# Optimization experiments

Measured on AMD Instinct MI355X. Metric: run time of the kernel, lower is better.

## Reference

```python
import jax, jax.numpy as jnp
import numpy as np

N_NODES = 50000
NEG_SLOPE = 0.2


def gat_layer(x, src, dst, edge_attr, W, a_src, a_dst, We, a_edge, b, n):
    """PyG GATConv (heads=1, concat=True, add_self_loops=True, fill_value='mean')."""
    h = x @ W                                   # [N, C] shared lin for src/dst
    alpha_s = h @ a_src                          # [N]
    alpha_d = h @ a_dst                          # [N]
    # self loops; self-loop edge_attr = mean of incoming edge_attr per node
    deg = jax.ops.segment_sum(jnp.ones_like(dst, dtype=edge_attr.dtype), dst, num_segments=n)
    ea_mean = jax.ops.segment_sum(edge_attr, dst, num_segments=n) / jnp.maximum(deg, 1.0)[:, None]
    loop = jnp.arange(n, dtype=src.dtype)
    s = jnp.concatenate([src, loop])             # [E+N]
    d = jnp.concatenate([dst, loop])
    ea = jnp.concatenate([edge_attr, ea_mean], axis=0)
    alpha_e = (ea @ We) @ a_edge                 # [E+N]
    alpha = jax.nn.leaky_relu(alpha_s[s] + alpha_d[d] + alpha_e, NEG_SLOPE)
    # segment softmax over destination neighborhoods (self-loops guarantee non-empty)
    amax = jax.ops.segment_max(alpha, d, num_segments=n)
    ealpha = jnp.exp(alpha - amax[d])
    denom = jax.ops.segment_sum(ealpha, d, num_segments=n)
    coef = ealpha / denom[d]                     # [E+N]
    out = jax.ops.segment_sum(h[s] * coef[:, None], d, num_segments=n)
    return out + b


def setup_inputs() -> dict:
    key = jax.random.key(0)
    ks = jax.random.split(key, 16)
    N, E, F_in, H, C, ED = N_NODES, 800000, 256, 128, 128, 60
    inp = {
        "x": jax.random.normal(ks[0], (N, F_in), jnp.float32),
        "edge_index": jax.random.randint(ks[1], (2, E), 0, N, jnp.int32),
        "edge_features": jax.random.normal(ks[2], (E, ED), jnp.float32),
        "batch_size": 16,
    }
    def glorot(k, shape):
        fan = shape[0] + (shape[1] if len(shape) > 1 else 1)
        return jax.random.normal(k, shape, jnp.float32) * np.sqrt(2.0 / fan)
    # layer 1
    inp["W1"] = glorot(ks[3], (F_in, H))
    inp["a_src1"] = glorot(ks[4], (H,))
    inp["a_dst1"] = glorot(ks[5], (H,))
    inp["We1"] = glorot(ks[6], (ED, H))
    inp["a_edge1"] = glorot(ks[7], (H,))
    inp["b1"] = jnp.zeros((H,), jnp.float32)
    # layer 2
    inp["W2"] = glorot(ks[8], (H, C))
    inp["a_src2"] = glorot(ks[9], (C,))
    inp["a_dst2"] = glorot(ks[10], (C,))
    inp["We2"] = glorot(ks[11], (ED, C))
    inp["a_edge2"] = glorot(ks[12], (C,))
    inp["b2"] = jnp.zeros((C,), jnp.float32)
    return inp


def reference(x, edge_index, edge_features, batch_size,
              W1, a_src1, a_dst1, We1, a_edge1, b1,
              W2, a_src2, a_dst2, We2, a_edge2, b2):
    n = x.shape[0]
    src, dst = edge_index[0], edge_index[1]
    h = gat_layer(x, src, dst, edge_features, W1, a_src1, a_dst1, We1, a_edge1, b1, n)
    h = jax.nn.relu(h)
    z = gat_layer(h, src, dst, edge_features, W2, a_src2, a_dst2, We2, a_edge2, b2, n)
    # decode: gather-dot over labeled edge pairs
    res = jnp.sum(z[src] * z[dst], axis=-1)      # [E]
    half = res.shape[0] // 2
    res_half = res[:half] + res[half:]
    return res_half.reshape((batch_size, -1))
```

## Files before the change

kernel.cpp:

```cpp
#include <hip/hip_runtime.h>
#include <hip/hip_bf16.h>

typedef __attribute__((ext_vector_type(8))) short short8;
typedef __attribute__((ext_vector_type(4))) float floatx4;

__device__ __forceinline__ float lrelu(float a){ return a > 0.f ? a : 0.2f * a; }
__device__ __forceinline__ float bflo(unsigned u){ return __uint_as_float(u << 16); }
__device__ __forceinline__ float bfhi(unsigned u){ return __uint_as_float(u & 0xffff0000u); }
__device__ __forceinline__ unsigned short f2bf(float f){
  __hip_bfloat16 h = __float2bfloat16(f);
  return *reinterpret_cast<unsigned short*>(&h);
}
__device__ __forceinline__ float dot4(float4 a, float4 b){
  return a.x*b.x + a.y*b.y + a.z*b.z + a.w*b.w;
}

__global__ __launch_bounds__(256) void k_prep(const int* __restrict__ dst, int* __restrict__ degi,
                       int* __restrict__ eslot, int E, int CB,
                       const float* __restrict__ We1, const float* __restrict__ ae1,
                       const float* __restrict__ We2, const float* __restrict__ ae2,
                       float* __restrict__ we1, float* __restrict__ we2,
                       const float* __restrict__ W1, unsigned short* __restrict__ W1t,
                       const float* __restrict__ W2, unsigned short* __restrict__ W2t) {
  int t = threadIdx.x;
  if (blockIdx.x < (unsigned)CB) {
    int e = blockIdx.x * 256 + t;
    if (e < E) eslot[e] = atomicAdd(degi + dst[e], 1);
    return;
  }
  int b = blockIdx.x - CB;
  if (b == 0) {
    if (t >= 64) return;
    float s1 = 0.f, s2 = 0.f;
    if (t < 60) {
      const float4* r1 = reinterpret_cast<const float4*>(We1 + t * 128);
      const float4* r2 = reinterpret_cast<const float4*>(We2 + t * 128);
      const float4* a1 = reinterpret_cast<const float4*>(ae1);
      const float4* a2 = reinterpret_cast<const float4*>(ae2);
      for (int i = 0; i < 32; ++i) {
        float4 x1 = r1[i], y1 = a1[i];
        float4 x2 = r2[i], y2 = a2[i];
        s1 += x1.x*y1.x + x1.y*y1.y + x1.z*y1.z + x1.w*y1.w;
        s2 += x2.x*y2.x + x2.y*y2.y + x2.z*y2.z + x2.w*y2.w;
      }
    }
    we1[t] = s1; we2[t] = s2;
  } else if (b <= 128) {
    int idx = (b - 1) * 256 + t;
    int k = idx >> 7, n = idx & 127;
    W1t[(size_t)n * 256 + k] = f2bf(W1[idx]);
  } else {
    int idx = (b - 129) * 256 + t;
    int k = idx >> 7, n = idx & 127;
    W2t[(size_t)n * 128 + k] = f2bf(W2[idx]);
  }
}

__device__ __forceinline__ void scan_body(const int* __restrict__ degi, int* __restrict__ rowptr,
                                          int N, int E) {
  __shared__ int wsums[16];
  int t = threadIdx.x;
  int wave = t >> 6, lane = t & 63;
  const int CH = 52;
  int lo = t * CH;
  int v[52];
  int s = 0;
  #pragma unroll
  for (int i = 0; i < 13; ++i) {
    int base_i = lo + 4 * i;
    if (base_i + 4 <= N) {
      int4 q = *reinterpret_cast<const int4*>(degi + base_i);
      v[4*i+0] = q.x; v[4*i+1] = q.y; v[4*i+2] = q.z; v[4*i+3] = q.w;
      s += q.x + q.y + q.z + q.w;
    } else {
      #pragma unroll
      for (int j = 0; j < 4; ++j) {
        int idx = base_i + j;
        int x = (idx < N) ? degi[idx] : 0;
        v[4*i+j] = x; s += x;
      }
    }
  }
  int inc = s;
  #pragma unroll
  for (int off = 1; off < 64; off <<= 1) {
    int u = __shfl_up(inc, off);
    if (lane >= off) inc += u;
  }
  if (lane == 63) wsums[wave] = inc;
  __syncthreads();
  if (wave == 0) {
    int ws = (lane < 16) ? wsums[lane] : 0;
    #pragma unroll
    for (int off = 1; off < 16; off <<= 1) {
      int u = __shfl_up(ws, off);
      if (lane >= off) ws += u;
    }
    if (lane < 16) wsums[lane] = ws;
  }
  __syncthreads();
  int base = inc - s + (wave ? wsums[wave - 1] : 0);
  #pragma unroll
  for (int i = 0; i < 13; ++i) {
    int base_i = lo + 4 * i;
    if (base_i + 4 <= N) {
      int4 o;
      o.x = base; base += v[4*i+0];
      o.y = base; base += v[4*i+1];
      o.z = base; base += v[4*i+2];
      o.w = base; base += v[4*i+3];
      *reinterpret_cast<int4*>(rowptr + base_i) = o;
    } else {
      #pragma unroll
      for (int j = 0; j < 4; ++j) {
        int idx = base_i + j;
        if (idx < N) { rowptr[idx] = base; base += v[4*i+j]; }
      }
    }
  }
  if (t == 0) rowptr[N] = E;
}

__global__ __launch_bounds__(1024) void k_scanedot(const int* __restrict__ degi, int* __restrict__ rowptr,
                       int N, int E,
                       const float* __restrict__ ef,
                       const float* __restrict__ we1, const float* __restrict__ we2,
                       float2* __restrict__ edgeD, int EDOTB) {
  if (blockIdx.x == 0) { scan_body(degi, rowptr, N, E); return; }
  int t = threadIdx.x;
  int sub = t & 3;
  int qw = (int)(blockIdx.x - 1) * 256 + (t >> 2);
  const float4* w1v = reinterpret_cast<const float4*>(we1);
  const float4* w2v = reinterpret_cast<const float4*>(we2);
  float4 wa0 = w1v[sub],     wb0 = w2v[sub];
  float4 wa1 = w1v[sub + 4], wb1 = w2v[sub + 4];
  float4 wa2 = w1v[sub + 8], wb2 = w2v[sub + 8];
  bool has3 = sub < 3;
  float4 wa3 = make_float4(0.f,0.f,0.f,0.f), wb3 = wa3;
  if (has3) { wa3 = w1v[sub + 12]; wb3 = w2v[sub + 12]; }
  const float4* efq = reinterpret_cast<const float4*>(ef);
  int stride = EDOTB * 256;
  for (int e = qw; e < E; e += stride) {
    size_t b = (size_t)e * 15;
    float4 f0 = efq[b + sub];
    float4 f1 = efq[b + sub + 4];
    float4 f2 = efq[b + sub + 8];
    float4 f3 = make_float4(0.f,0.f,0.f,0.f);
    if (has3) f3 = efq[b + sub + 12];
    float d1 = dot4(f0, wa0) + dot4(f1, wa1) + dot4(f2, wa2) + dot4(f3, wa3);
    float d2 = dot4(f0, wb0) + dot4(f1, wb1) + dot4(f2, wb2) + dot4(f3, wb3);
    d1 += __shfl_xor(d1, 1); d1 += __shfl_xor(d1, 2);
    d2 += __shfl_xor(d2, 1); d2 += __shfl_xor(d2, 2);
    if (sub == 0) edgeD[e] = make_float2(d1, d2);
  }
}

template <int K, bool AFP32>
__device__ __forceinline__ void gemm_body(int wid, int lane,
    const void* __restrict__ Av, const unsigned short* __restrict__ Bt,
    unsigned short* __restrict__ C,
    const float* __restrict__ a_src, const float* __restrict__ a_dst,
    float* __restrict__ alps, float* __restrict__ alpd, int M) {
  int mt = wid;
  if (mt * 16 >= M) return;
  int r = lane & 15, quad = lane >> 4;
  int m = mt * 16 + r;
  floatx4 acc[8] = {};
  for (int k0 = 0; k0 < K; k0 += 32) {
    int kk = k0 + quad * 8;
    short8 a;
    if (AFP32) {
      const float4* ap = reinterpret_cast<const float4*>((const float*)Av + (size_t)m * K + kk);
      float4 lo = ap[0], hi = ap[1];
      union { short8 v; unsigned short u[8]; } pa;
      pa.u[0]=f2bf(lo.x); pa.u[1]=f2bf(lo.y); pa.u[2]=f2bf(lo.z); pa.u[3]=f2bf(lo.w);
      pa.u[4]=f2bf(hi.x); pa.u[5]=f2bf(hi.y); pa.u[6]=f2bf(hi.z); pa.u[7]=f2bf(hi.w);
      a = pa.v;
    } else {
      a = *reinterpret_cast<const short8*>((const unsigned short*)Av + (size_t)m * K + kk);
    }
    #pragma unroll
    for (int t = 0; t < 8; ++t) {
      short8 b = *reinterpret_cast<const short8*>(Bt + (size_t)(t*16 + r) * K + kk);
      acc[t] = __builtin_amdgcn_mfma_f32_16x16x32_bf16(a, b, acc[t], 0, 0, 0);
    }
  }
  float asv[8], adv[8];
  #pragma unroll
  for (int t = 0; t < 8; ++t) {
    int col = t * 16 + r;
    asv[t] = a_src[col]; adv[t] = a_dst[col];
  }
  #pragma unroll
  for (int rr = 0; rr < 4; ++rr) {
    float ps = 0.f, pd = 0.f;
    #pragma unroll
    for (int t = 0; t < 8; ++t) { ps += acc[t][rr] * asv[t]; pd += acc[t][rr] * adv[t]; }
    #pragma unroll
    for (int mo = 1; mo <= 8; mo <<= 1) { ps += __shfl_xor(ps, mo); pd += __shfl_xor(pd, mo); }
    if (r == 0) {
      int row = mt * 16 + quad * 4 + rr;
      alps[row] = ps;
      alpd[row] = pd;
    }
  }
  #pragma unroll
  for (int t = 0; t < 8; ++t) {
    int col = t * 16 + r;
    #pragma unroll
    for (int rr = 0; rr < 4; ++rr) {
      int row = mt * 16 + quad * 4 + rr;
      C[(size_t)row * 128 + col] = f2bf(acc[t][rr]);
    }
  }
}

template <int K, bool AFP32>
__global__ __launch_bounds__(256) void k_gemm(const void* __restrict__ Av, const unsigned short* __restrict__ Bt,
                                              unsigned short* __restrict__ C,
                                              const float* __restrict__ a_src, const float* __restrict__ a_dst,
                                              float* __restrict__ alps, float* __restrict__ alpd, int M) {
  int wid = (blockIdx.x * 256 + threadIdx.x) >> 6;
  int lane = threadIdx.x & 63;
  gemm_body<K, AFP32>(wid, lane, Av, Bt, C, a_src, a_dst, alps, alpd, M);
}

__global__ __launch_bounds__(256) void k_scatgemm(
                       const int* __restrict__ src, const int* __restrict__ dst,
                       const int* __restrict__ eslot, const int* __restrict__ rowptr,
                       const float2* __restrict__ edgeD, float4* __restrict__ csr,
                       int E, int GB,
                       const float* __restrict__ x, const unsigned short* __restrict__ W1t,
                       unsigned short* __restrict__ hA,
                       const float* __restrict__ a_src, const float* __restrict__ a_dst,
                       float* __restrict__ alps, float* __restrict__ alpd, int N) {
  int t = threadIdx.x;
  if (blockIdx.x < (unsigned)GB) {
    int wid = (blockIdx.x * 256 + t) >> 6;
    int lane = t & 63;
    gemm_body<256, true>(wid, lane, x, W1t, hA, a_src, a_dst, alps, alpd, N);
    return;
  }
  int e = (blockIdx.x - GB) * 256 + t;
  if (e >= E) return;
  int d = dst[e];
  float2 dd = edgeD[e];
  int slot = rowptr[d] + eslot[e];
  float4 v;
  v.x = __int_as_float(src[e]); v.y = dd.x; v.z = dd.y; v.w = 0.f;
  csr[slot] = v;
}

__global__ __launch_bounds__(256) void k_agg(const int* __restrict__ rowptr, const float4* __restrict__ csr,
                      const float* __restrict__ as_, const float* __restrict__ ad_,
                      const unsigned short* __restrict__ h, const float* __restrict__ bias,
                      unsigned short* __restrict__ out, int N, int use2, int do_relu) {
  int i = (blockIdx.x * blockDim.x + threadIdx.x) >> 6;
  int lane = threadIdx.x & 63;
  if (i >= N) return;
  int st = lane >> 4;
  int q  = lane & 15;
  int start = rowptr[i], end = rowptr[i + 1];
  int cnt = end - start;
  float adi = ad_[i], asi = as_[i];
  float m = -3.0e38f, s = 0.f, esum = 0.f;
  float acc[8] = {};
  int idx = start + st;
  float4 cur, nx;
  float as_c = 0.f; uint4 hv_c;
  if (idx < end) {
    cur = csr[idx];
    int sv = __float_as_int(cur.x);
    as_c = as_[sv];
    hv_c = *reinterpret_cast<const uint4*>(h + (size_t)sv * 128 + q * 8);
  }
  if (idx + 4 < end) nx = csr[idx + 4];
  for (; idx < end; idx += 4) {
    float4 n2;
    if (idx + 8 < end) n2 = csr[idx + 8];
    float as_n = 0.f; uint4 hv_n;
    if (idx + 4 < end) {
      int svn = __float_as_int(nx.x);
      as_n = as_[svn];
      hv_n = *reinterpret_cast<const uint4*>(h + (size_t)svn * 128 + q * 8);
    }
    float e = use2 ? cur.z : cur.y;
    float a = lrelu(as_c + adi + e);
    esum += e;
    if (a > m + 8.f) {
      float rr = __expf(m - a);
      s *= rr;
      #pragma unroll
      for (int j = 0; j < 8; ++j) acc[j] *= rr;
      m = a;
    }
    float w = __expf(a - m);
    s += w;
    acc[0] += w * bflo(hv_c.x); acc[1] += w * bfhi(hv_c.x);
    acc[2] += w * bflo(hv_c.y); acc[3] += w * bfhi(hv_c.y);
    acc[4] += w * bflo(hv_c.z); acc[5] += w * bfhi(hv_c.z);
    acc[6] += w * bflo(hv_c.w); acc[7] += w * bfhi(hv_c.w);
    cur = nx; nx = n2; as_c = as_n; hv_c = hv_n;
  }
  #pragma unroll
  for (int off = 16; off <= 32; off <<= 1) {
    float m_o = __shfl_xor(m, off);
    float s_o = __shfl_xor(s, off);
    float e_o = __shfl_xor(esum, off);
    float ao[8];
    #pragma unroll
    for (int j = 0; j < 8; ++j) ao[j] = __shfl_xor(acc[j], off);
    float Mn = fmaxf(m, m_o);
    float f  = __expf(m - Mn), fo = __expf(m_o - Mn);
    s = s * f + s_o * fo;
    #pragma unroll
    for (int j = 0; j < 8; ++j) acc[j] = acc[j] * f + ao[j] * fo;
    esum += e_o;
    m = Mn;
  }
  float a_self = lrelu(asi + adi + esum / fmaxf((float)cnt, 1.f));
  float M2 = fmaxf(m, a_self);
  float g = __expf(m - M2);
  float w_self = __expf(a_self - M2);
  s = s * g + w_self;
  uint4 hs = *reinterpret_cast<const uint4*>(h + (size_t)i * 128 + q * 8);
  float hsf[8] = { bflo(hs.x), bfhi(hs.x), bflo(hs.y), bfhi(hs.y),
                   bflo(hs.z), bfhi(hs.z), bflo(hs.w), bfhi(hs.w) };
  #pragma unroll
  for (int j = 0; j < 8; ++j) acc[j] = acc[j] * g + w_self * hsf[j];
  float inv = 1.0f / s;
  float4 bv0 = *reinterpret_cast<const float4*>(bias + q * 8);
  float4 bv1 = *reinterpret_cast<const float4*>(bias + q * 8 + 4);
  float o[8];
  o[0] = acc[0]*inv + bv0.x; o[1] = acc[1]*inv + bv0.y;
  o[2] = acc[2]*inv + bv0.z; o[3] = acc[3]*inv + bv0.w;
  o[4] = acc[4]*inv + bv1.x; o[5] = acc[5]*inv + bv1.y;
  o[6] = acc[6]*inv + bv1.z; o[7] = acc[7]*inv + bv1.w;
  if (do_relu) {
    #pragma unroll
    for (int j = 0; j < 8; ++j) o[j] = fmaxf(o[j], 0.f);
  }
  if (st == 0) {
    uint4 ov;
    ov.x = (unsigned)f2bf(o[0]) | ((unsigned)f2bf(o[1]) << 16);
    ov.y = (unsigned)f2bf(o[2]) | ((unsigned)f2bf(o[3]) << 16);
    ov.z = (unsigned)f2bf(o[4]) | ((unsigned)f2bf(o[5]) << 16);
    ov.w = (unsigned)f2bf(o[6]) | ((unsigned)f2bf(o[7]) << 16);
    *reinterpret_cast<uint4*>(out + (size_t)i * 128 + q * 8) = ov;
  }
}

__global__ void k_decode(const int* __restrict__ src, const int* __restrict__ dst,
                         const unsigned short* __restrict__ z, float* __restrict__ out, int halfE) {
  int w = (blockIdx.x * blockDim.x + threadIdx.x) >> 6;
  int lane = threadIdx.x & 63;
  int k0 = w * 4;
  if (k0 >= halfE) return;
  int g = lane >> 3;
  int q = lane & 7;
  int r = g >> 1, hh = g & 1;
  int k = k0 + r;
  float p = 0.f;
  if (k < halfE) {
    int e = k + hh * halfE;
    int sv = src[e], dv = dst[e];
    const uint4* za = reinterpret_cast<const uint4*>(z + (size_t)sv * 128 + q * 16);
    const uint4* zb = reinterpret_cast<const uint4*>(z + (size_t)dv * 128 + q * 16);
    uint4 a0 = za[0], a1 = za[1];
    uint4 b0 = zb[0], b1 = zb[1];
    p = bflo(a0.x)*bflo(b0.x) + bfhi(a0.x)*bfhi(b0.x)
      + bflo(a0.y)*bflo(b0.y) + bfhi(a0.y)*bfhi(b0.y)
      + bflo(a0.z)*bflo(b0.z) + bfhi(a0.z)*bfhi(b0.z)
      + bflo(a0.w)*bflo(b0.w) + bfhi(a0.w)*bfhi(b0.w)
      + bflo(a1.x)*bflo(b1.x) + bfhi(a1.x)*bfhi(b1.x)
      + bflo(a1.y)*bflo(b1.y) + bfhi(a1.y)*bfhi(b1.y)
      + bflo(a1.z)*bflo(b1.z) + bfhi(a1.z)*bfhi(b1.z)
      + bflo(a1.w)*bflo(b1.w) + bfhi(a1.w)*bfhi(b1.w);
  }
  p += __shfl_xor(p, 1);
  p += __shfl_xor(p, 2);
  p += __shfl_xor(p, 4);
  p += __shfl_xor(p, 8);
  if ((lane & 15) == 0) {
    int kk = k0 + (lane >> 4);
    if (kk < halfE) out[kk] = p;
  }
}

extern "C" void kernel_launch(void* const* d_in, const int* in_sizes, int n_in,
                              void* d_out, int out_size, void* d_ws, size_t ws_size,
                              hipStream_t stream) {
  const int H = 128;
  const int N = in_sizes[0] / 256;
  const int E = in_sizes[1] / 2;
  const int half = E / 2;

  const float* x   = (const float*)d_in[0];
  const int* eidx  = (const int*)d_in[1];
  const float* ef  = (const float*)d_in[2];
  const float* W1  = (const float*)d_in[4];
  const float* as1 = (const float*)d_in[5];
  const float* ad1 = (const float*)d_in[6];
  const float* We1 = (const float*)d_in[7];
  const float* ae1 = (const float*)d_in[8];
  const float* b1  = (const float*)d_in[9];
  const float* W2  = (const float*)d_in[10];
  const float* as2 = (const float*)d_in[11];
  const float* ad2 = (const float*)d_in[12];
  const float* We2 = (const float*)d_in[13];
  const float* ae2 = (const float*)d_in[14];
  const float* b2  = (const float*)d_in[15];

  const int* src = eidx;
  const int* dst = eidx + E;

  size_t off = 0;
  auto alloc = [&](size_t bytes) -> void* {
    void* p = (char*)d_ws + off;
    off += (bytes + 255) & ~(size_t)255;
    return p;
  };
  float*  we1    = (float*)alloc(64 * 4);
  float*  we2    = (float*)alloc(64 * 4);
  int*    degi   = (int*)alloc((size_t)N * 4);
  float*  alps   = (float*)alloc((size_t)N * 4);
  float*  alpd   = (float*)alloc((size_t)N * 4);
  int*    eslot  = (int*)alloc((size_t)E * 4);
  int*    rowptr = (int*)alloc((size_t)(N + 1) * 4);
  float2* edgeD  = (float2*)alloc((size_t)E * 8);
  float4* csr    = (float4*)alloc((size_t)E * 16);
  unsigned short* W1t = (unsigned short*)alloc((size_t)128 * 256 * 2);
  unsigned short* W2t = (unsigned short*)alloc((size_t)128 * 128 * 2);
  unsigned short* hA  = (unsigned short*)alloc((size_t)N * H * 2);
  unsigned short* hB  = (unsigned short*)alloc((size_t)N * H * 2);

  hipMemsetAsync(degi, 0, (size_t)N * 4, stream);

  int CB = (E + 255) / 256;
  k_prep<<<CB + 193, 256, 0, stream>>>(dst, degi, eslot, E, CB,
                                       We1, ae1, We2, ae2, we1, we2, W1, W1t, W2, W2t);

  int EDOTB = 782;
  k_scanedot<<<1 + EDOTB, 1024, 0, stream>>>(degi, rowptr, N, E, ef, we1, we2, edgeD, EDOTB);

  int gwaves = (N + 15) / 16;
  int GB = (gwaves + 3) / 4;
  int SB = (E + 255) / 256;
  k_scatgemm<<<GB + SB, 256, 0, stream>>>(src, dst, eslot, rowptr, edgeD, csr, E, GB,
                                          x, W1t, hA, as1, ad1, alps, alpd, N);
  k_agg<<<(N + 3) / 4, 256, 0, stream>>>(rowptr, csr, alps, alpd, hA, b1, hB, N, 0, 1);
  k_gemm<128, false><<<GB, 256, 0, stream>>>(hB, W2t, hA, as2, ad2, alps, alpd, N);
  k_agg<<<(N + 3) / 4, 256, 0, stream>>>(rowptr, csr, alps, alpd, hA, b2, hB, N, 1, 0);
  int dwaves = (half + 3) / 4;
  k_decode<<<(dwaves + 3) / 4, 256, 0, stream>>>(src, dst, hB, (float*)d_out, half);
}
```

Measured before the change: 562.4 us.

## Decode edges in source-sorted order and deepen prefetch in aggregation

Builds a second counting sort of the edges by source node: atomic counts, a second scan block and a scatter into packed (src, dst, output index) records. The decode kernel then walks edges in source order, so gathers of the source rows hit cache more often. Each edge's score is accumulated into a zeroed output with a float atomic add, which also folds the two halves together. In exchange this adds atomics, an extra scan and a scatter pass, and makes the summation order nondeterministic. The aggregation loop is also changed to prefetch two edges ahead instead of one, to hide more gather latency.

Measured after the change: 605.4 us. +7.6%, slower.

```diff
diff --git a/kernel.cpp b/kernel.cpp
--- a/kernel.cpp
+++ b/kernel.cpp
@@ -15,8 +15,9 @@
   return a.x*b.x + a.y*b.y + a.z*b.z + a.w*b.w;
 }
 
-__global__ __launch_bounds__(256) void k_prep(const int* __restrict__ dst, int* __restrict__ degi,
-                       int* __restrict__ eslot, int E, int CB,
+__global__ __launch_bounds__(256) void k_prep(const int* __restrict__ src, const int* __restrict__ dst,
+                       int* __restrict__ degi, int* __restrict__ sdeg,
+                       int* __restrict__ eslot, int* __restrict__ sslot, int E, int CB,
                        const float* __restrict__ We1, const float* __restrict__ ae1,
                        const float* __restrict__ We2, const float* __restrict__ ae2,
                        float* __restrict__ we1, float* __restrict__ we2,
@@ -25,7 +26,10 @@
   int t = threadIdx.x;
   if (blockIdx.x < (unsigned)CB) {
     int e = blockIdx.x * 256 + t;
-    if (e < E) eslot[e] = atomicAdd(degi + dst[e], 1);
+    if (e < E) {
+      eslot[e] = atomicAdd(degi + dst[e], 1);
+      sslot[e] = atomicAdd(sdeg + src[e], 1);
+    }
     return;
   }
   int b = blockIdx.x - CB;
@@ -122,14 +126,16 @@
 }
 
 __global__ __launch_bounds__(1024) void k_scanedot(const int* __restrict__ degi, int* __restrict__ rowptr,
+                       const int* __restrict__ sdeg, int* __restrict__ srowptr,
                        int N, int E,
                        const float* __restrict__ ef,
                        const float* __restrict__ we1, const float* __restrict__ we2,
                        float2* __restrict__ edgeD, int EDOTB) {
   if (blockIdx.x == 0) { scan_body(degi, rowptr, N, E); return; }
+  if (blockIdx.x == 1) { scan_body(sdeg, srowptr, N, E); return; }
   int t = threadIdx.x;
   int sub = t & 3;
-  int qw = (int)(blockIdx.x - 1) * 256 + (t >> 2);
+  int qw = (int)(blockIdx.x - 2) * 256 + (t >> 2);
   const float4* w1v = reinterpret_cast<const float4*>(we1);
   const float4* w2v = reinterpret_cast<const float4*>(we2);
   float4 wa0 = w1v[sub],     wb0 = w2v[sub];
@@ -228,8 +234,10 @@
 __global__ __launch_bounds__(256) void k_scatgemm(
                        const int* __restrict__ src, const int* __restrict__ dst,
                        const int* __restrict__ eslot, const int* __restrict__ rowptr,
+                       const int* __restrict__ sslot, const int* __restrict__ srowptr,
                        const float2* __restrict__ edgeD, float4* __restrict__ csr,
-                       int E, int GB,
+                       uint2* __restrict__ sedge,
+                       int E, int half, int GB,
                        const float* __restrict__ x, const unsigned short* __restrict__ W1t,
                        unsigned short* __restrict__ hA,
                        const float* __restrict__ a_src, const float* __restrict__ a_dst,
@@ -243,12 +251,18 @@
   }
   int e = (blockIdx.x - GB) * 256 + t;
   if (e >= E) return;
-  int d = dst[e];
+  int s = src[e], d = dst[e];
   float2 dd = edgeD[e];
   int slot = rowptr[d] + eslot[e];
   float4 v;
-  v.x = __int_as_float(src[e]); v.y = dd.x; v.z = dd.y; v.w = 0.f;
+  v.x = __int_as_float(s); v.y = dd.x; v.z = dd.y; v.w = 0.f;
   csr[slot] = v;
+  int ss = srowptr[s] + sslot[e];
+  int outidx = (e < half) ? e : e - half;
+  uint2 rec;
+  rec.x = (unsigned)s | ((unsigned)d << 16);
+  rec.y = (unsigned)outidx;
+  sedge[ss] = rec;
 }
 
 __global__ __launch_bounds__(256) void k_agg(const int* __restrict__ rowptr, const float4* __restrict__ csr,
@@ -266,23 +280,30 @@
   float m = -3.0e38f, s = 0.f, esum = 0.f;
   float acc[8] = {};
   int idx = start + st;
-  float4 cur, nx;
-  float as_c = 0.f; uint4 hv_c;
+  float4 cur, nx1, nx2;
+  float as_c = 0.f, as_1 = 0.f;
+  uint4 hv_c, hv_1;
+  if (idx < end) cur = csr[idx];
+  if (idx + 4 < end) nx1 = csr[idx + 4];
+  if (idx + 8 < end) nx2 = csr[idx + 8];
   if (idx < end) {
-    cur = csr[idx];
     int sv = __float_as_int(cur.x);
     as_c = as_[sv];
     hv_c = *reinterpret_cast<const uint4*>(h + (size_t)sv * 128 + q * 8);
   }
-  if (idx + 4 < end) nx = csr[idx + 4];
+  if (idx + 4 < end) {
+    int sv = __float_as_int(nx1.x);
+    as_1 = as_[sv];
+    hv_1 = *reinterpret_cast<const uint4*>(h + (size_t)sv * 128 + q * 8);
+  }
   for (; idx < end; idx += 4) {
-    float4 n2;
-    if (idx + 8 < end) n2 = csr[idx + 8];
-    float as_n = 0.f; uint4 hv_n;
-    if (idx + 4 < end) {
-      int svn = __float_as_int(nx.x);
-      as_n = as_[svn];
-      hv_n = *reinterpret_cast<const uint4*>(h + (size_t)svn * 128 + q * 8);
+    float4 n3;
+    if (idx + 12 < end) n3 = csr[idx + 12];
+    float as_2 = 0.f; uint4 hv_2;
+    if (idx + 8 < end) {
+      int sv = __float_as_int(nx2.x);
+      as_2 = as_[sv];
+      hv_2 = *reinterpret_cast<const uint4*>(h + (size_t)sv * 128 + q * 8);
     }
     float e = use2 ? cur.z : cur.y;
     float a = lrelu(as_c + adi + e);
@@ -300,7 +321,9 @@
     acc[2] += w * bflo(hv_c.y); acc[3] += w * bfhi(hv_c.y);
     acc[4] += w * bflo(hv_c.z); acc[5] += w * bfhi(hv_c.z);
     acc[6] += w * bflo(hv_c.w); acc[7] += w * bfhi(hv_c.w);
-    cur = nx; nx = n2; as_c = as_n; hv_c = hv_n;
+    cur = nx1; nx1 = nx2; nx2 = n3;
+    as_c = as_1; hv_c = hv_1;
+    as_1 = as_2; hv_1 = hv_2;
   }
   #pragma unroll
   for (int off = 16; off <= 32; off <<= 1) {
@@ -350,41 +373,30 @@
   }
 }
 
-__global__ void k_decode(const int* __restrict__ src, const int* __restrict__ dst,
-                         const unsigned short* __restrict__ z, float* __restrict__ out, int halfE) {
-  int w = (blockIdx.x * blockDim.x + threadIdx.x) >> 6;
-  int lane = threadIdx.x & 63;
-  int k0 = w * 4;
-  if (k0 >= halfE) return;
-  int g = lane >> 3;
-  int q = lane & 7;
-  int r = g >> 1, hh = g & 1;
-  int k = k0 + r;
-  float p = 0.f;
-  if (k < halfE) {
-    int e = k + hh * halfE;
-    int sv = src[e], dv = dst[e];
-    const uint4* za = reinterpret_cast<const uint4*>(z + (size_t)sv * 128 + q * 16);
-    const uint4* zb = reinterpret_cast<const uint4*>(z + (size_t)dv * 128 + q * 16);
-    uint4 a0 = za[0], a1 = za[1];
-    uint4 b0 = zb[0], b1 = zb[1];
-    p = bflo(a0.x)*bflo(b0.x) + bfhi(a0.x)*bfhi(b0.x)
-      + bflo(a0.y)*bflo(b0.y) + bfhi(a0.y)*bfhi(b0.y)
-      + bflo(a0.z)*bflo(b0.z) + bfhi(a0.z)*bfhi(b0.z)
-      + bflo(a0.w)*bflo(b0.w) + bfhi(a0.w)*bfhi(b0.w)
-      + bflo(a1.x)*bflo(b1.x) + bfhi(a1.x)*bfhi(b1.x)
-      + bflo(a1.y)*bflo(b1.y) + bfhi(a1.y)*bfhi(b1.y)
-      + bflo(a1.z)*bflo(b1.z) + bfhi(a1.z)*bfhi(b1.z)
-      + bflo(a1.w)*bflo(b1.w) + bfhi(a1.w)*bfhi(b1.w);
-  }
+__global__ __launch_bounds__(256) void k_decode_sorted(const uint2* __restrict__ sedge,
+                         const unsigned short* __restrict__ z, float* __restrict__ out, int E) {
+  int j = (blockIdx.x * 256 + threadIdx.x) >> 3;
+  if (j >= E) return;
+  int q = threadIdx.x & 7;
+  uint2 rec = sedge[j];
+  int s = rec.x & 0xffff;
+  int d = rec.x >> 16;
+  const uint4* za = reinterpret_cast<const uint4*>(z + (size_t)s * 128 + q * 16);
+  const uint4* zb = reinterpret_cast<const uint4*>(z + (size_t)d * 128 + q * 16);
+  uint4 a0 = za[0], a1 = za[1];
+  uint4 b0 = zb[0], b1 = zb[1];
+  float p = bflo(a0.x)*bflo(b0.x) + bfhi(a0.x)*bfhi(b0.x)
+          + bflo(a0.y)*bflo(b0.y) + bfhi(a0.y)*bfhi(b0.y)
+          + bflo(a0.z)*bflo(b0.z) + bfhi(a0.z)*bfhi(b0.z)
+          + bflo(a0.w)*bflo(b0.w) + bfhi(a0.w)*bfhi(b0.w)
+          + bflo(a1.x)*bflo(b1.x) + bfhi(a1.x)*bfhi(b1.x)
+          + bflo(a1.y)*bflo(b1.y) + bfhi(a1.y)*bfhi(b1.y)
+          + bflo(a1.z)*bflo(b1.z) + bfhi(a1.z)*bfhi(b1.z)
+          + bflo(a1.w)*bflo(b1.w) + bfhi(a1.w)*bfhi(b1.w);
   p += __shfl_xor(p, 1);
   p += __shfl_xor(p, 2);
   p += __shfl_xor(p, 4);
-  p += __shfl_xor(p, 8);
-  if ((lane & 15) == 0) {
-    int kk = k0 + (lane >> 4);
-    if (kk < halfE) out[kk] = p;
-  }
+  if (q == 0) atomicAdd(out + rec.y, p);
 }
 
 extern "C" void kernel_launch(void* const* d_in, const int* in_sizes, int n_in,
@@ -422,35 +434,43 @@
   };
   float*  we1    = (float*)alloc(64 * 4);
   float*  we2    = (float*)alloc(64 * 4);
-  int*    degi   = (int*)alloc((size_t)N * 4);
+  int*    degs   = (int*)alloc((size_t)N * 4 * 2);
+  int*    degi   = degs;
+  int*    sdeg   = degs + N;
   float*  alps   = (float*)alloc((size_t)N * 4);
   float*  alpd   = (float*)alloc((size_t)N * 4);
   int*    eslot  = (int*)alloc((size_t)E * 4);
+  int*    sslot  = (int*)alloc((size_t)E * 4);
   int*    rowptr = (int*)alloc((size_t)(N + 1) * 4);
+  int*    srowptr= (int*)alloc((size_t)(N + 1) * 4);
   float2* edgeD  = (float2*)alloc((size_t)E * 8);
   float4* csr    = (float4*)alloc((size_t)E * 16);
+  uint2*  sedge  = (uint2*)alloc((size_t)E * 8);
   unsigned short* W1t = (unsigned short*)alloc((size_t)128 * 256 * 2);
   unsigned short* W2t = (unsigned short*)alloc((size_t)128 * 128 * 2);
   unsigned short* hA  = (unsigned short*)alloc((size_t)N * H * 2);
   unsigned short* hB  = (unsigned short*)alloc((size_t)N * H * 2);
 
-  hipMemsetAsync(degi, 0, (size_t)N * 4, stream);
+  hipMemsetAsync(degs, 0, (size_t)N * 8, stream);
+  hipMemsetAsync(d_out, 0, (size_t)out_size, stream);
 
   int CB = (E + 255) / 256;
-  k_prep<<<CB + 193, 256, 0, stream>>>(dst, degi, eslot, E, CB,
+  k_prep<<<CB + 193, 256, 0, stream>>>(src, dst, degi, sdeg, eslot, sslot, E, CB,
                                        We1, ae1, We2, ae2, we1, we2, W1, W1t, W2, W2t);
 
   int EDOTB = 782;
-  k_scanedot<<<1 + EDOTB, 1024, 0, stream>>>(degi, rowptr, N, E, ef, we1, we2, edgeD, EDOTB);
+  k_scanedot<<<2 + EDOTB, 1024, 0, stream>>>(degi, rowptr, sdeg, srowptr, N, E,
+                                             ef, we1, we2, edgeD, EDOTB);
 
   int gwaves = (N + 15) / 16;
   int GB = (gwaves + 3) / 4;
   int SB = (E + 255) / 256;
-  k_scatgemm<<<GB + SB, 256, 0, stream>>>(src, dst, eslot, rowptr, edgeD, csr, E, GB,
+  k_scatgemm<<<GB + SB, 256, 0, stream>>>(src, dst, eslot, rowptr, sslot, srowptr,
+                                          edgeD, csr, sedge, E, half, GB,
                                           x, W1t, hA, as1, ad1, alps, alpd, N);
   k_agg<<<(N + 3) / 4, 256, 0, stream>>>(rowptr, csr, alps, alpd, hA, b1, hB, N, 0, 1);
   k_gemm<128, false><<<GB, 256, 0, stream>>>(hB, W2t, hA, as2, ad2, alps, alpd, N);
   k_agg<<<(N + 3) / 4, 256, 0, stream>>>(rowptr, csr, alps, alpd, hA, b2, hB, N, 1, 0);
-  int dwaves = (half + 3) / 4;
-  k_decode<<<(dwaves + 3) / 4, 256, 0, stream>>>(src, dst, hB, (float*)d_out, half);
-}
+  int DB = (E * 8 + 255) / 256;
+  k_decode_sorted<<<DB, 256, 0, stream>>>(sedge, hB, (float*)d_out, E);
+}
```

## Use two wavefronts per node in aggregation with LDS merge of softmax partials

Applied to the files above, without the earlier changes.

The aggregation kernel now assigns two 64-lane wavefronts (8 edge streams) to each destination node instead of one wavefront (4 streams). The two waves' online-softmax partials are merged through shared memory after a block barrier. The intent is to double the memory-level parallelism of the neighbour gathers, since each node averages about 16 incoming edges. The cost is twice as many threads per node, an added __syncthreads, LDS traffic, and idle lanes on low-degree nodes.

New measurement: 579.5 us. 1.03x slower.

```diff
diff --git a/kernel.cpp b/kernel.cpp
--- a/kernel.cpp
+++ b/kernel.cpp
@@ -255,14 +255,19 @@
                       const float* __restrict__ as_, const float* __restrict__ ad_,
                       const unsigned short* __restrict__ h, const float* __restrict__ bias,
                       unsigned short* __restrict__ out, int N, int use2, int do_relu) {
-  int i = (blockIdx.x * blockDim.x + threadIdx.x) >> 6;
-  int lane = threadIdx.x & 63;
-  if (i >= N) return;
-  int st = lane >> 4;
+  __shared__ float mrg[2][16][11];
+  int tid = threadIdx.x;
+  int nb = tid >> 7;
+  int i = blockIdx.x * 2 + nb;
+  int wv = (tid >> 6) & 1;
+  int lane = tid & 63;
+  int st = wv * 4 + (lane >> 4);
   int q  = lane & 15;
-  int start = rowptr[i], end = rowptr[i + 1];
+  bool valid = i < N;
+  int start = 0, end = 0;
+  float adi = 0.f, asi = 0.f;
+  if (valid) { start = rowptr[i]; end = rowptr[i + 1]; adi = ad_[i]; asi = as_[i]; }
   int cnt = end - start;
-  float adi = ad_[i], asi = as_[i];
   float m = -3.0e38f, s = 0.f, esum = 0.f;
   float acc[8] = {};
   int idx = start + st;
@@ -274,12 +279,12 @@
     as_c = as_[sv];
     hv_c = *reinterpret_cast<const uint4*>(h + (size_t)sv * 128 + q * 8);
   }
-  if (idx + 4 < end) nx = csr[idx + 4];
-  for (; idx < end; idx += 4) {
+  if (idx + 8 < end) nx = csr[idx + 8];
+  for (; idx < end; idx += 8) {
     float4 n2;
-    if (idx + 8 < end) n2 = csr[idx + 8];
+    if (idx + 16 < end) n2 = csr[idx + 16];
     float as_n = 0.f; uint4 hv_n;
-    if (idx + 4 < end) {
+    if (idx + 8 < end) {
       int svn = __float_as_int(nx.x);
       as_n = as_[svn];
       hv_n = *reinterpret_cast<const uint4*>(h + (size_t)svn * 128 + q * 8);
@@ -315,6 +320,25 @@
     s = s * f + s_o * fo;
     #pragma unroll
     for (int j = 0; j < 8; ++j) acc[j] = acc[j] * f + ao[j] * fo;
+    esum += e_o;
+    m = Mn;
+  }
+  if (wv == 1 && lane < 16) {
+    mrg[nb][q][0] = m; mrg[nb][q][1] = s; mrg[nb][q][2] = esum;
+    #pragma unroll
+    for (int j = 0; j < 8; ++j) mrg[nb][q][3 + j] = acc[j];
+  }
+  __syncthreads();
+  if (wv != 0 || !valid) return;
+  {
+    float m_o = mrg[nb][q][0];
+    float s_o = mrg[nb][q][1];
+    float e_o = mrg[nb][q][2];
+    float Mn = fmaxf(m, m_o);
+    float f  = __expf(m - Mn), fo = __expf(m_o - Mn);
+    s = s * f + s_o * fo;
+    #pragma unroll
+    for (int j = 0; j < 8; ++j) acc[j] = acc[j] * f + mrg[nb][q][3 + j] * fo;
     esum += e_o;
     m = Mn;
   }
@@ -340,7 +364,7 @@
     #pragma unroll
     for (int j = 0; j < 8; ++j) o[j] = fmaxf(o[j], 0.f);
   }
-  if (st == 0) {
+  if (lane < 16) {
     uint4 ov;
     ov.x = (unsigned)f2bf(o[0]) | ((unsigned)f2bf(o[1]) << 16);
     ov.y = (unsigned)f2bf(o[2]) | ((unsigned)f2bf(o[3]) << 16);
@@ -448,9 +472,9 @@
   int SB = (E + 255) / 256;
   k_scatgemm<<<GB + SB, 256, 0, stream>>>(src, dst, eslot, rowptr, edgeD, csr, E, GB,
                                           x, W1t, hA, as1, ad1, alps, alpd, N);
-  k_agg<<<(N + 3) / 4, 256, 0, stream>>>(rowptr, csr, alps, alpd, hA, b1, hB, N, 0, 1);
+  k_agg<<<(N + 1) / 2, 256, 0, stream>>>(rowptr, csr, alps, alpd, hA, b1, hB, N, 0, 1);
   k_gemm<128, false><<<GB, 256, 0, stream>>>(hB, W2t, hA, as2, ad2, alps, alpd, N);
-  k_agg<<<(N + 3) / 4, 256, 0, stream>>>(rowptr, csr, alps, alpd, hA, b2, hB, N, 1, 0);
+  k_agg<<<(N + 1) / 2, 256, 0, stream>>>(rowptr, csr, alps, alpd, hA, b2, hB, N, 1, 0);
   int dwaves = (half + 3) / 4;
   k_decode<<<(dwaves + 3) / 4, 256, 0, stream>>>(src, dst, hB, (float*)d_out, half);
 }
```

## Move edge-dot into prep kernel and deepen gather prefetch in aggregation

Applied to the files above, without the earlier changes.

The per-edge attention-feature dot product moves out of the scan kernel into the prep kernel. Each block recomputes the We·a_edge vectors in shared memory, so the edge-dot no longer waits on a separate reduction step and runs alongside the degree atomics and weight transposes. The scan becomes its own single-block kernel. The aggregation loop now prefetches CSR entries and source features two iterations ahead instead of one, hiding gather latency at the cost of extra registers.

Result: no change. 558.1 us (-0.8%).

```diff
diff --git a/kernel.cpp b/kernel.cpp
--- a/kernel.cpp
+++ b/kernel.cpp
@@ -15,49 +15,85 @@
   return a.x*b.x + a.y*b.y + a.z*b.z + a.w*b.w;
 }
 
-__global__ __launch_bounds__(256) void k_prep(const int* __restrict__ dst, int* __restrict__ degi,
-                       int* __restrict__ eslot, int E, int CB,
+__global__ __launch_bounds__(256) void k_prep(
+                       const int* __restrict__ dst, int* __restrict__ degi,
+                       int* __restrict__ eslot, int E, int EDOTB, int CB,
                        const float* __restrict__ We1, const float* __restrict__ ae1,
                        const float* __restrict__ We2, const float* __restrict__ ae2,
-                       float* __restrict__ we1, float* __restrict__ we2,
+                       const float* __restrict__ ef, float2* __restrict__ edgeD,
                        const float* __restrict__ W1, unsigned short* __restrict__ W1t,
                        const float* __restrict__ W2, unsigned short* __restrict__ W2t) {
   int t = threadIdx.x;
-  if (blockIdx.x < (unsigned)CB) {
-    int e = blockIdx.x * 256 + t;
+  unsigned b = blockIdx.x;
+  if (b < (unsigned)EDOTB) {
+    __shared__ float4 lw1v[16], lw2v[16];
+    float* lw1 = reinterpret_cast<float*>(lw1v);
+    float* lw2 = reinterpret_cast<float*>(lw2v);
+    if (t < 64) {
+      float s = 0.f;
+      if (t < 60) {
+        const float4* r = reinterpret_cast<const float4*>(We1 + t * 128);
+        const float4* a = reinterpret_cast<const float4*>(ae1);
+        for (int i = 0; i < 32; ++i) { float4 x = r[i], y = a[i];
+          s += x.x*y.x + x.y*y.y + x.z*y.z + x.w*y.w; }
+      }
+      lw1[t] = s;
+    } else if (t < 128) {
+      int k = t - 64;
+      float s = 0.f;
+      if (k < 60) {
+        const float4* r = reinterpret_cast<const float4*>(We2 + k * 128);
+        const float4* a = reinterpret_cast<const float4*>(ae2);
+        for (int i = 0; i < 32; ++i) { float4 x = r[i], y = a[i];
+          s += x.x*y.x + x.y*y.y + x.z*y.z + x.w*y.w; }
+      }
+      lw2[k] = s;
+    }
+    __syncthreads();
+    int sub = t & 3;
+    int qg = (int)b * 64 + (t >> 2);
+    float4 wa0 = lw1v[sub],     wb0 = lw2v[sub];
+    float4 wa1 = lw1v[sub + 4], wb1 = lw2v[sub + 4];
+    float4 wa2 = lw1v[sub + 8], wb2 = lw2v[sub + 8];
+    bool has3 = sub < 3;
+    float4 wa3 = make_float4(0.f,0.f,0.f,0.f), wb3 = wa3;
+    if (has3) { wa3 = lw1v[sub + 12]; wb3 = lw2v[sub + 12]; }
+    const float4* efq = reinterpret_cast<const float4*>(ef);
+    int stride = EDOTB * 64;
+    for (int e = qg; e < E; e += stride) {
+      size_t bb = (size_t)e * 15;
+      float4 f0 = efq[bb + sub];
+      float4 f1 = efq[bb + sub + 4];
+      float4 f2 = efq[bb + sub + 8];
+      float4 f3 = make_float4(0.f,0.f,0.f,0.f);
+      if (has3) f3 = efq[bb + sub + 12];
+      float d1 = dot4(f0, wa0) + dot4(f1, wa1) + dot4(f2, wa2) + dot4(f3, wa3);
+      float d2 = dot4(f0, wb0) + dot4(f1, wb1) + dot4(f2, wb2) + dot4(f3, wb3);
+      d1 += __shfl_xor(d1, 1); d1 += __shfl_xor(d1, 2);
+      d2 += __shfl_xor(d2, 1); d2 += __shfl_xor(d2, 2);
+      if (sub == 0) edgeD[e] = make_float2(d1, d2);
+    }
+    return;
+  }
+  if (b < (unsigned)(EDOTB + CB)) {
+    int e = (b - EDOTB) * 256 + t;
     if (e < E) eslot[e] = atomicAdd(degi + dst[e], 1);
     return;
   }
-  int b = blockIdx.x - CB;
-  if (b == 0) {
-    if (t >= 64) return;
-    float s1 = 0.f, s2 = 0.f;
-    if (t < 60) {
-      const float4* r1 = reinterpret_cast<const float4*>(We1 + t * 128);
-      const float4* r2 = reinterpret_cast<const float4*>(We2 + t * 128);
-      const float4* a1 = reinterpret_cast<const float4*>(ae1);
-      const float4* a2 = reinterpret_cast<const float4*>(ae2);
-      for (int i = 0; i < 32; ++i) {
-        float4 x1 = r1[i], y1 = a1[i];
-        float4 x2 = r2[i], y2 = a2[i];
-        s1 += x1.x*y1.x + x1.y*y1.y + x1.z*y1.z + x1.w*y1.w;
-        s2 += x2.x*y2.x + x2.y*y2.y + x2.z*y2.z + x2.w*y2.w;
-      }
-    }
-    we1[t] = s1; we2[t] = s2;
-  } else if (b <= 128) {
-    int idx = (b - 1) * 256 + t;
+  int bb = b - EDOTB - CB;
+  if (bb < 128) {
+    int idx = bb * 256 + t;
     int k = idx >> 7, n = idx & 127;
     W1t[(size_t)n * 256 + k] = f2bf(W1[idx]);
   } else {
-    int idx = (b - 129) * 256 + t;
+    int idx = (bb - 128) * 256 + t;
     int k = idx >> 7, n = idx & 127;
     W2t[(size_t)n * 128 + k] = f2bf(W2[idx]);
   }
 }
 
-__device__ __forceinline__ void scan_body(const int* __restrict__ degi, int* __restrict__ rowptr,
-                                          int N, int E) {
+__global__ __launch_bounds__(1024) void k_scan(const int* __restrict__ degi, int* __restrict__ rowptr,
+                                               int N, int E) {
   __shared__ int wsums[16];
   int t = threadIdx.x;
   int wave = t >> 6, lane = t & 63;
@@ -119,40 +155,6 @@
     }
   }
   if (t == 0) rowptr[N] = E;
-}
-
-__global__ __launch_bounds__(1024) void k_scanedot(const int* __restrict__ degi, int* __restrict__ rowptr,
-                       int N, int E,
-                       const float* __restrict__ ef,
-                       const float* __restrict__ we1, const float* __restrict__ we2,
-                       float2* __restrict__ edgeD, int EDOTB) {
-  if (blockIdx.x == 0) { scan_body(degi, rowptr, N, E); return; }
-  int t = threadIdx.x;
-  int sub = t & 3;
-  int qw = (int)(blockIdx.x - 1) * 256 + (t >> 2);
-  const float4* w1v = reinterpret_cast<const float4*>(we1);
-  const float4* w2v = reinterpret_cast<const float4*>(we2);
-  float4 wa0 = w1v[sub],     wb0 = w2v[sub];
-  float4 wa1 = w1v[sub + 4], wb1 = w2v[sub + 4];
-  float4 wa2 = w1v[sub + 8], wb2 = w2v[sub + 8];
-  bool has3 = sub < 3;
-  float4 wa3 = make_float4(0.f,0.f,0.f,0.f), wb3 = wa3;
-  if (has3) { wa3 = w1v[sub + 12]; wb3 = w2v[sub + 12]; }
-  const float4* efq = reinterpret_cast<const float4*>(ef);
-  int stride = EDOTB * 256;
-  for (int e = qw; e < E; e += stride) {
-    size_t b = (size_t)e * 15;
-    float4 f0 = efq[b + sub];
-    float4 f1 = efq[b + sub + 4];
-    float4 f2 = efq[b + sub + 8];
-    float4 f3 = make_float4(0.f,0.f,0.f,0.f);
-    if (has3) f3 = efq[b + sub + 12];
-    float d1 = dot4(f0, wa0) + dot4(f1, wa1) + dot4(f2, wa2) + dot4(f3, wa3);
-    float d2 = dot4(f0, wb0) + dot4(f1, wb1) + dot4(f2, wb2) + dot4(f3, wb3);
-    d1 += __shfl_xor(d1, 1); d1 += __shfl_xor(d1, 2);
-    d2 += __shfl_xor(d2, 1); d2 += __shfl_xor(d2, 2);
-    if (sub == 0) edgeD[e] = make_float2(d1, d2);
-  }
 }
 
 template <int K, bool AFP32>
@@ -266,23 +268,30 @@
   float m = -3.0e38f, s = 0.f, esum = 0.f;
   float acc[8] = {};
   int idx = start + st;
-  float4 cur, nx;
-  float as_c = 0.f; uint4 hv_c;
+  float4 cur, nx1, nx2;
+  float as_c = 0.f, as_1 = 0.f;
+  uint4 hv_c, hv_1;
+  if (idx < end) cur = csr[idx];
+  if (idx + 4 < end) nx1 = csr[idx + 4];
+  if (idx + 8 < end) nx2 = csr[idx + 8];
   if (idx < end) {
-    cur = csr[idx];
     int sv = __float_as_int(cur.x);
     as_c = as_[sv];
     hv_c = *reinterpret_cast<const uint4*>(h + (size_t)sv * 128 + q * 8);
   }
-  if (idx + 4 < end) nx = csr[idx + 4];
+  if (idx + 4 < end) {
+    int sv = __float_as_int(nx1.x);
+    as_1 = as_[sv];
+    hv_1 = *reinterpret_cast<const uint4*>(h + (size_t)sv * 128 + q * 8);
+  }
   for (; idx < end; idx += 4) {
-    float4 n2;
-    if (idx + 8 < end) n2 = csr[idx + 8];
-    float as_n = 0.f; uint4 hv_n;
-    if (idx + 4 < end) {
-      int svn = __float_as_int(nx.x);
-      as_n = as_[svn];
-      hv_n = *reinterpret_cast<const uint4*>(h + (size_t)svn * 128 + q * 8);
+    float4 n3;
+    if (idx + 12 < end) n3 = csr[idx + 12];
+    float as_2 = 0.f; uint4 hv_2;
+    if (idx + 8 < end) {
+      int sv = __float_as_int(nx2.x);
+      as_2 = as_[sv];
+      hv_2 = *reinterpret_cast<const uint4*>(h + (size_t)sv * 128 + q * 8);
     }
     float e = use2 ? cur.z : cur.y;
     float a = lrelu(as_c + adi + e);
@@ -300,7 +309,9 @@
     acc[2] += w * bflo(hv_c.y); acc[3] += w * bfhi(hv_c.y);
     acc[4] += w * bflo(hv_c.z); acc[5] += w * bfhi(hv_c.z);
     acc[6] += w * bflo(hv_c.w); acc[7] += w * bfhi(hv_c.w);
-    cur = nx; nx = n2; as_c = as_n; hv_c = hv_n;
+    cur = nx1; nx1 = nx2; nx2 = n3;
+    as_c = as_1; hv_c = hv_1;
+    as_1 = as_2; hv_1 = hv_2;
   }
   #pragma unroll
   for (int off = 16; off <= 32; off <<= 1) {
@@ -420,8 +431,6 @@
     off += (bytes + 255) & ~(size_t)255;
     return p;
   };
-  float*  we1    = (float*)alloc(64 * 4);
-  float*  we2    = (float*)alloc(64 * 4);
   int*    degi   = (int*)alloc((size_t)N * 4);
   float*  alps   = (float*)alloc((size_t)N * 4);
   float*  alpd   = (float*)alloc((size_t)N * 4);
@@ -437,11 +446,11 @@
   hipMemsetAsync(degi, 0, (size_t)N * 4, stream);
 
   int CB = (E + 255) / 256;
-  k_prep<<<CB + 193, 256, 0, stream>>>(dst, degi, eslot, E, CB,
-                                       We1, ae1, We2, ae2, we1, we2, W1, W1t, W2, W2t);
-
-  int EDOTB = 782;
-  k_scanedot<<<1 + EDOTB, 1024, 0, stream>>>(degi, rowptr, N, E, ef, we1, we2, edgeD, EDOTB);
+  int EDOTB = 3125;
+  k_prep<<<EDOTB + CB + 192, 256, 0, stream>>>(dst, degi, eslot, E, EDOTB, CB,
+                                               We1, ae1, We2, ae2, ef, edgeD,
+                                               W1, W1t, W2, W2t);
+  k_scan<<<1, 1024, 0, stream>>>(degi, rowptr, N, E);
 
   int gwaves = (N + 15) / 16;
   int GB = (gwaves + 3) / 4;
```
